# Optimization experiments

Measured on AMD Instinct MI355X. Metric: run time of the kernel, lower is better.

Reference implementation:

```python
import jax, jax.numpy as jnp
import numpy as np


def setup_inputs() -> dict:
    key = jax.random.key(0)
    ks = jax.random.split(key, 9)
    B, T, S, D = 4, 256, 256, 512
    scale = 1.0 / np.sqrt(D)
    inp = {
        "output": jax.random.normal(ks[0], (B, T, D), dtype=jnp.float32),
        "context": jax.random.normal(ks[1], (B, S, D), dtype=jnp.float32),
        "mask": jax.random.randint(ks[2], (B, S), 0, 2, dtype=jnp.int32),
        # learned params (nn.Linear stores y = x @ W.T + b; we store W.T directly)
        "Wq": jax.random.normal(ks[3], (D, D), dtype=jnp.float32) * scale,
        "bq": jax.random.normal(ks[4], (D,), dtype=jnp.float32) * scale,
        "Wc": jax.random.normal(ks[5], (D, D), dtype=jnp.float32) * scale,
        "v": jax.random.normal(ks[6], (D,), dtype=jnp.float32) * scale,
        "Wout": jax.random.normal(ks[7], (2 * D, D), dtype=jnp.float32) * scale,
        "bout": jax.random.normal(ks[8], (D,), dtype=jnp.float32) * scale,
    }
    return inp


def reference(output, context, mask, Wq, bq, Wc, v, Wout, bout):
    # output: (B, T, D) decoder states; context: (B, S, D) encoder states
    wq = jnp.einsum("btd,de->bte", output, Wq) + bq          # (B, T, D)
    uh = jnp.einsum("bsd,de->bse", context, Wc)               # (B, S, D)
    # additive score: v . tanh(wq + uh), broadcast over (T, S)
    wquh = jnp.tanh(wq[:, :, None, :] + uh[:, None, :, :])    # (B, T, S, D)
    score = jnp.einsum("btsd,d->bts", wquh, v)                # (B, T, S)
    # masked softmax exactly as the torch code: max over ALL positions,
    # then zero out masked entries (mask==1 means masked) and renormalize.
    max_by_row = jnp.max(score, axis=-1, keepdims=True)
    keep = (1.0 - mask.astype(score.dtype))[:, None, :]       # (B, 1, S)
    attn = jnp.exp(score - max_by_row) * keep
    attn = attn / jnp.sum(attn, axis=-1, keepdims=True)       # (B, T, S)
    mix = jnp.einsum("bts,bsd->btd", attn, context)           # (B, T, D)
    combined = jnp.concatenate([mix, output], axis=-1)        # (B, T, 2D)
    out = jnp.einsum("btf,fd->btd", combined, Wout) + bout    # (B, T, D)
    return out, attn
```

## Files before the change

### kernel.cpp

```cpp
#include <hip/hip_runtime.h>
#include <hip/hip_bf16.h>

#define B_ 4
#define T_ 256
#define S_ 256
#define D_ 512
#define TB 2

typedef __bf16 bf16x8 __attribute__((ext_vector_type(8)));
typedef float  floatx4 __attribute__((ext_vector_type(4)));

#define C2F 2.885390081777926f

static __device__ __forceinline__ unsigned short f2bf(float x) {
    __hip_bfloat16 h = __float2bfloat16(x);
    return *reinterpret_cast<unsigned short*>(&h);
}
static __device__ __forceinline__ float asf(unsigned int u) {
    float f; __builtin_memcpy(&f, &u, 4); return f;
}


__global__ __launch_bounds__(256) void prep(
    const float* __restrict__ output, const float* __restrict__ context,
    const float* __restrict__ Wq, const float* __restrict__ Wc,
    const float* __restrict__ Wout,
    unsigned short* __restrict__ out_f, unsigned short* __restrict__ ctx_f,
    unsigned short* __restrict__ Wq_f, unsigned short* __restrict__ Wc_f,
    unsigned short* __restrict__ WoT_f, unsigned short* __restrict__ WoB_f)
{
    const int tid = threadIdx.x;
    const int z = blockIdx.z;

    if (z >= 4) {
        const float* src = (z == 4) ? output : context;
        unsigned short* dst = (z == 4) ? out_f : ctx_f;
        const int bid  = blockIdx.y * 16 + blockIdx.x;
        const int tile = bid * 4 + (tid >> 6);
        const int lane = tid & 63;
        const int mblk = tile >> 4, kblk = tile & 15;
        const float* s = src + (size_t)(mblk * 16 + (lane & 15)) * 512
                             + kblk * 32 + (lane >> 4) * 8;
        float4 a = *(const float4*)s;
        float4 b = *(const float4*)(s + 4);
        uint4 pk;
        pk.x = (unsigned)f2bf(a.x) | ((unsigned)f2bf(a.y) << 16);
        pk.y = (unsigned)f2bf(a.z) | ((unsigned)f2bf(a.w) << 16);
        pk.z = (unsigned)f2bf(b.x) | ((unsigned)f2bf(b.y) << 16);
        pk.w = (unsigned)f2bf(b.z) | ((unsigned)f2bf(b.w) << 16);
        *(uint4*)(dst + (size_t)tile * 512 + lane * 8) = pk;
        return;
    }

    const float* W; unsigned short* WF; int krow0;
    if      (z == 0) { W = Wq;   WF = Wq_f;  krow0 = 0;   }
    else if (z == 1) { W = Wc;   WF = Wc_f;  krow0 = 0;   }
    else if (z == 2) { W = Wout; WF = WoT_f; krow0 = 0;   }
    else             { W = Wout; WF = WoB_f; krow0 = 512; }

    const int n0 = blockIdx.x * 32;
    const int k0 = blockIdx.y * 32;

    __shared__ float tile[32][33];
    const int c = tid & 31, r = tid >> 5;
    #pragma unroll
    for (int i = 0; i < 4; ++i)
        tile[r + 8 * i][c] = W[(size_t)(krow0 + k0 + r + 8 * i) * 512 + n0 + c];
    __syncthreads();
    #pragma unroll
    for (int i = 0; i < 4; ++i) {
        const int n = n0 + r + 8 * i;
        const int k = k0 + c;
        const int tl = (n >> 4) * 16 + (k >> 5);
        const int ln = (n & 15) | (((k >> 3) & 3) << 4);
        WF[((size_t)tl * 64 + ln) * 8 + (k & 7)] = f2bf(tile[c][r + 8 * i]);
    }
}

struct GArgs {
    const unsigned short* Af;
    const unsigned short* Bf;
    const float* aux;
    void* C;
    int mode;
};

__global__ __launch_bounds__(256) void gemm2(GArgs g0, GArgs g1, GArgs g2, GArgs g3)
{
    const int z = blockIdx.z;
    GArgs g = (z == 0) ? g0 : (z == 1) ? g1 : (z == 2) ? g2 : g3;

    const int tid  = threadIdx.x;
    const int wave = tid >> 6, lane = tid & 63;
    const int l15  = lane & 15, quad = lane >> 4;
    const int mblk = blockIdx.y * 4 + wave;
    const int nb0  = blockIdx.x * 2;

    const unsigned short* Ap  = g.Af + ((size_t)mblk * 16 * 64 + lane) * 8;
    const unsigned short* Bp0 = g.Bf + ((size_t)nb0 * 16 * 64 + lane) * 8;
    const unsigned short* Bp1 = Bp0 + (size_t)16 * 64 * 8;

    floatx4 acc[2];
    acc[0] = (floatx4){0.f, 0.f, 0.f, 0.f};
    acc[1] = (floatx4){0.f, 0.f, 0.f, 0.f};

    #pragma unroll 4
    for (int k = 0; k < 16; ++k) {
        bf16x8 a  = *(const bf16x8*)(Ap  + k * 512);
        bf16x8 b0 = *(const bf16x8*)(Bp0 + k * 512);
        bf16x8 b1 = *(const bf16x8*)(Bp1 + k * 512);
        acc[0] = __builtin_amdgcn_mfma_f32_16x16x32_bf16(a, b0, acc[0], 0, 0, 0);
        acc[1] = __builtin_amdgcn_mfma_f32_16x16x32_bf16(a, b1, acc[1], 0, 0, 0);
    }

    #pragma unroll
    for (int ni = 0; ni < 2; ++ni) {
        const int col = (nb0 + ni) * 16 + l15;
        const int rbase = mblk * 16 + quad * 4;
        if (g.mode == 3) {
            unsigned short* Cb = (unsigned short*)g.C;
            #pragma unroll
            for (int r = 0; r < 4; ++r) {
                int row = rbase + r, bb = row >> 8, ss = row & 255;
                Cb[((size_t)(bb * 64 + (col >> 3)) * 256 + ss) * 8 + (col & 7)]
                    = f2bf(C2F * acc[ni][r]);
            }
        } else if (g.mode == 5) {
            unsigned short* Cb = (unsigned short*)g.C;
            #pragma unroll
            for (int r = 0; r < 4; ++r)
                Cb[(size_t)(rbase + r) * 512 + col] = f2bf(acc[ni][r]);
        } else {
            float* Cf = (float*)g.C;
            float bv = g.aux ? g.aux[col] : 0.0f;
            #pragma unroll
            for (int r = 0; r < 4; ++r) {
                float val = acc[ni][r] + bv;
                if (g.mode == 1) val *= C2F;
                Cf[(size_t)(rbase + r) * 512 + col] = val;
            }
        }
    }
}

__global__ __launch_bounds__(1024) void attn_fused(
    const float* __restrict__ wqs,
    const unsigned short* __restrict__ uhb,
    const unsigned short* __restrict__ CWb,
    const float* __restrict__ OB,
    const int*   __restrict__ mask,
    const float* __restrict__ v,
    float* __restrict__ attn_out,
    float* __restrict__ out)
{
    const int bg  = blockIdx.x;
    const int b   = bg / (T_ / TB);
    const int t0  = (bg % (T_ / TB)) * TB;
    const int tid = threadIdx.x;
    const int s   = tid & 255;
    const int h   = tid >> 8;

    __shared__ float  w_s[TB][D_];
    __shared__ float  v_s[D_];
    __shared__ float2 part[4][256];
    __shared__ float2 wred[4];
    __shared__ float  a_s[TB][256];
    __shared__ float  mixp[4][TB][D_];

    if (tid < 512) {
        w_s[0][tid] = wqs[(size_t)(b * T_ + t0 + 0) * D_ + tid];
        w_s[1][tid] = wqs[(size_t)(b * T_ + t0 + 1) * D_ + tid];
        v_s[tid]    = v[tid];
    }
    __syncthreads();

    float acc0 = 0.f, acc1 = 0.f;
    const int dd0 = h * 16;
    const uint4* u4 = (const uint4*)(uhb + ((size_t)(b * 64 + dd0) * 256 + s) * 8);

    #pragma unroll 4
    for (int dd = 0; dd < 16; ++dd) {
        uint4 uu = u4[(size_t)dd * 256];
        float uf[8];
        uf[0] = asf(uu.x << 16); uf[1] = asf(uu.x & 0xffff0000u);
        uf[2] = asf(uu.y << 16); uf[3] = asf(uu.y & 0xffff0000u);
        uf[4] = asf(uu.z << 16); uf[5] = asf(uu.z & 0xffff0000u);
        uf[6] = asf(uu.w << 16); uf[7] = asf(uu.w & 0xffff0000u);

        const int dbase = (dd0 + dd) * 8;
        #pragma unroll
        for (int j = 0; j < 8; ++j) {
            float vv = v_s[dbase + j];
            float x0 = w_s[0][dbase + j] + uf[j];
            float x1 = w_s[1][dbase + j] + uf[j];
            float r0 = __builtin_amdgcn_rcpf(__builtin_amdgcn_exp2f(x0) + 1.0f);
            float r1 = __builtin_amdgcn_rcpf(__builtin_amdgcn_exp2f(x1) + 1.0f);
            acc0 = fmaf(vv, r0, acc0);
            acc1 = fmaf(vv, r1, acc1);
        }
    }
    part[h][s] = make_float2(acc0, acc1);
    __syncthreads();

    float p0 = 0.f, p1 = 0.f;
    if (tid < 256) {
        float A0 = part[0][tid].x + part[1][tid].x + part[2][tid].x + part[3][tid].x;
        float A1 = part[0][tid].y + part[1][tid].y + part[2][tid].y + part[3][tid].y;
        float keep = 1.0f - (float)mask[b * S_ + tid];
        p0 = __builtin_amdgcn_exp2f(-C2F * A0) * keep;
        p1 = __builtin_amdgcn_exp2f(-C2F * A1) * keep;
        float s0 = p0, s1 = p1;
        #pragma unroll
        for (int off = 1; off < 64; off <<= 1) {
            s0 += __shfl_xor(s0, off);
            s1 += __shfl_xor(s1, off);
        }
        if ((tid & 63) == 0) wred[tid >> 6] = make_float2(s0, s1);
    }
    __syncthreads();

    if (tid < 256) {
        float den0 = wred[0].x + wred[1].x + wred[2].x + wred[3].x;
        float den1 = wred[0].y + wred[1].y + wred[2].y + wred[3].y;
        float a0 = p0 * __builtin_amdgcn_rcpf(den0);
        float a1 = p1 * __builtin_amdgcn_rcpf(den1);
        attn_out[(size_t)(b * T_ + t0 + 0) * S_ + tid] = a0;
        attn_out[(size_t)(b * T_ + t0 + 1) * S_ + tid] = a1;
        a_s[0][tid] = a0;
        a_s[1][tid] = a1;
    }
    __syncthreads();

    const int d2 = tid & 255;
    const int sh = h * 64;
    const unsigned short* cw = CWb + ((size_t)(b * S_) + sh) * D_ + 2 * d2;
    float m[TB][2] = {};
    #pragma unroll 8
    for (int s2 = 0; s2 < 64; ++s2) {
        unsigned int cc = *(const unsigned int*)(cw + (size_t)s2 * D_);
        float c0 = asf(cc << 16), c1 = asf(cc & 0xffff0000u);
        #pragma unroll
        for (int t = 0; t < TB; ++t) {
            float a = a_s[t][sh + s2];
            m[t][0] = fmaf(a, c0, m[t][0]);
            m[t][1] = fmaf(a, c1, m[t][1]);
        }
    }
    #pragma unroll
    for (int t = 0; t < TB; ++t) {
        mixp[h][t][2 * d2]     = m[t][0];
        mixp[h][t][2 * d2 + 1] = m[t][1];
    }
    __syncthreads();

    {
        const int t = tid >> 9, d = tid & 511;
        size_t idx = (size_t)(b * T_ + t0 + t) * D_ + d;
        out[idx] = mixp[0][t][d] + mixp[1][t][d] + mixp[2][t][d] + mixp[3][t][d]
                 + OB[idx];
    }
}

extern "C" void kernel_launch(void* const* d_in, const int* in_sizes, int n_in,
                              void* d_out, int out_size, void* d_ws, size_t ws_size,
                              hipStream_t stream) {
    const float* output  = (const float*)d_in[0];
    const float* context = (const float*)d_in[1];
    const int*   mask    = (const int*)d_in[2];
    const float* Wq      = (const float*)d_in[3];
    const float* bq      = (const float*)d_in[4];
    const float* Wc      = (const float*)d_in[5];
    const float* v       = (const float*)d_in[6];
    const float* Wout    = (const float*)d_in[7];
    const float* bout    = (const float*)d_in[8];

    float* out  = (float*)d_out;
    float* attn = out + (size_t)B_ * T_ * D_;

    char* ws = (char*)d_ws;
    float* wqs           = (float*)ws;
    float* OB            = (float*)(ws + (2u << 20));
    unsigned short* uhb   = (unsigned short*)(ws + (4u << 20));
    unsigned short* out_f = (unsigned short*)(ws + (5u << 20));
    unsigned short* ctx_f = (unsigned short*)(ws + (6u << 20));
    unsigned short* Wq_f  = (unsigned short*)(ws + (7u << 20));
    unsigned short* Wc_f  = (unsigned short*)(ws + (7u << 20) + (512u << 10));
    unsigned short* WoT_f = (unsigned short*)(ws + (8u << 20));
    unsigned short* WoB_f = (unsigned short*)(ws + (8u << 20) + (512u << 10));
    unsigned short* CWb   = (unsigned short*)(ws + (9u << 20));

    dim3 blk(256);

    prep<<<dim3(16, 16, 6), blk, 0, stream>>>(
        output, context, Wq, Wc, Wout, out_f, ctx_f, Wq_f, Wc_f, WoT_f, WoB_f);

    GArgs gwq = { out_f, Wq_f,  bq,      wqs, 1 };
    GArgs guh = { ctx_f, Wc_f,  nullptr, uhb, 3 };
    GArgs gob = { out_f, WoB_f, bout,    OB,  4 };
    GArgs gcw = { ctx_f, WoT_f, nullptr, CWb, 5 };
    gemm2<<<dim3(16, 16, 4), blk, 0, stream>>>(gwq, guh, gob, gcw);

    attn_fused<<<dim3(B_ * T_ / TB), dim3(1024), 0, stream>>>(
        wqs, uhb, CWb, OB, mask, v, attn, out);
}
```

Measured before the change: 122.0 us.

## Fuse bf16 conversion into GEMM with LDS-staged 64x64 tiles, drop prep kernel

Removes the separate prep kernel that converted activations and weights to bf16 fragment layout. The GEMM now loads fp32 inputs directly, converts them to bf16 while staging into shared memory, and computes 64x64 tiles per block with a 2x2 wave layout. This saves one launch and the workspace round trip, at the cost of redundant conversion across blocks and uncoalesced strided weight-column loads with no double buffering.

Result: no change. 124.3 us (+1.8%).

```diff
diff --git a/kernel.cpp b/kernel.cpp
--- a/kernel.cpp
+++ b/kernel.cpp
@@ -20,124 +20,112 @@
     float f; __builtin_memcpy(&f, &u, 4); return f;
 }
 
-
-__global__ __launch_bounds__(256) void prep(
-    const float* __restrict__ output, const float* __restrict__ context,
-    const float* __restrict__ Wq, const float* __restrict__ Wc,
-    const float* __restrict__ Wout,
-    unsigned short* __restrict__ out_f, unsigned short* __restrict__ ctx_f,
-    unsigned short* __restrict__ Wq_f, unsigned short* __restrict__ Wc_f,
-    unsigned short* __restrict__ WoT_f, unsigned short* __restrict__ WoB_f)
-{
-    const int tid = threadIdx.x;
-    const int z = blockIdx.z;
-
-    if (z >= 4) {
-        const float* src = (z == 4) ? output : context;
-        unsigned short* dst = (z == 4) ? out_f : ctx_f;
-        const int bid  = blockIdx.y * 16 + blockIdx.x;
-        const int tile = bid * 4 + (tid >> 6);
-        const int lane = tid & 63;
-        const int mblk = tile >> 4, kblk = tile & 15;
-        const float* s = src + (size_t)(mblk * 16 + (lane & 15)) * 512
-                             + kblk * 32 + (lane >> 4) * 8;
-        float4 a = *(const float4*)s;
-        float4 b = *(const float4*)(s + 4);
-        uint4 pk;
-        pk.x = (unsigned)f2bf(a.x) | ((unsigned)f2bf(a.y) << 16);
-        pk.y = (unsigned)f2bf(a.z) | ((unsigned)f2bf(a.w) << 16);
-        pk.z = (unsigned)f2bf(b.x) | ((unsigned)f2bf(b.y) << 16);
-        pk.w = (unsigned)f2bf(b.z) | ((unsigned)f2bf(b.w) << 16);
-        *(uint4*)(dst + (size_t)tile * 512 + lane * 8) = pk;
-        return;
-    }
-
-    const float* W; unsigned short* WF; int krow0;
-    if      (z == 0) { W = Wq;   WF = Wq_f;  krow0 = 0;   }
-    else if (z == 1) { W = Wc;   WF = Wc_f;  krow0 = 0;   }
-    else if (z == 2) { W = Wout; WF = WoT_f; krow0 = 0;   }
-    else             { W = Wout; WF = WoB_f; krow0 = 512; }
-
-    const int n0 = blockIdx.x * 32;
-    const int k0 = blockIdx.y * 32;
-
-    __shared__ float tile[32][33];
-    const int c = tid & 31, r = tid >> 5;
-    #pragma unroll
-    for (int i = 0; i < 4; ++i)
-        tile[r + 8 * i][c] = W[(size_t)(krow0 + k0 + r + 8 * i) * 512 + n0 + c];
-    __syncthreads();
-    #pragma unroll
-    for (int i = 0; i < 4; ++i) {
-        const int n = n0 + r + 8 * i;
-        const int k = k0 + c;
-        const int tl = (n >> 4) * 16 + (k >> 5);
-        const int ln = (n & 15) | (((k >> 3) & 3) << 4);
-        WF[((size_t)tl * 64 + ln) * 8 + (k & 7)] = f2bf(tile[c][r + 8 * i]);
-    }
-}
-
-struct GArgs {
-    const unsigned short* Af;
-    const unsigned short* Bf;
+struct G3 {
+    const float* A;
+    const float* W;
+    int krow0;
     const float* aux;
     void* C;
     int mode;
 };
 
-__global__ __launch_bounds__(256) void gemm2(GArgs g0, GArgs g1, GArgs g2, GArgs g3)
+__global__ __launch_bounds__(256) void gemm3(G3 g0, G3 g1, G3 g2, G3 g3)
 {
     const int z = blockIdx.z;
-    GArgs g = (z == 0) ? g0 : (z == 1) ? g1 : (z == 2) ? g2 : g3;
+    G3 g = (z == 0) ? g0 : (z == 1) ? g1 : (z == 2) ? g2 : g3;
 
     const int tid  = threadIdx.x;
     const int wave = tid >> 6, lane = tid & 63;
     const int l15  = lane & 15, quad = lane >> 4;
-    const int mblk = blockIdx.y * 4 + wave;
-    const int nb0  = blockIdx.x * 2;
-
-    const unsigned short* Ap  = g.Af + ((size_t)mblk * 16 * 64 + lane) * 8;
-    const unsigned short* Bp0 = g.Bf + ((size_t)nb0 * 16 * 64 + lane) * 8;
-    const unsigned short* Bp1 = Bp0 + (size_t)16 * 64 * 8;
-
-    floatx4 acc[2];
-    acc[0] = (floatx4){0.f, 0.f, 0.f, 0.f};
-    acc[1] = (floatx4){0.f, 0.f, 0.f, 0.f};
-
-    #pragma unroll 4
-    for (int k = 0; k < 16; ++k) {
-        bf16x8 a  = *(const bf16x8*)(Ap  + k * 512);
-        bf16x8 b0 = *(const bf16x8*)(Bp0 + k * 512);
-        bf16x8 b1 = *(const bf16x8*)(Bp1 + k * 512);
-        acc[0] = __builtin_amdgcn_mfma_f32_16x16x32_bf16(a, b0, acc[0], 0, 0, 0);
-        acc[1] = __builtin_amdgcn_mfma_f32_16x16x32_bf16(a, b1, acc[1], 0, 0, 0);
-    }
-
+    const int wm   = wave >> 1, wn = wave & 1;
+    const int m0   = blockIdx.y * 64;
+    const int n0   = blockIdx.x * 64;
+
+    __shared__ unsigned short Af[4 * 64 * 8];
+    __shared__ unsigned short Bf[4 * 64 * 8];
+
+    const int sm  = tid >> 2, skq = tid & 3;
+    const int sn  = tid & 63, sk8 = (tid >> 6) * 8;
+
+    const float* Abase = g.A + (size_t)(m0 + sm) * 512 + skq * 8;
+    const float* Wbase = g.W + (size_t)(g.krow0 + sk8) * 512 + n0 + sn;
+
+    unsigned short* Awr = Af + ((size_t)(sm >> 4) * 64 + ((sm & 15) | (skq << 4))) * 8;
+    unsigned short* Bwr = Bf + ((size_t)(sn >> 4) * 64 + ((sn & 15) | ((sk8 >> 3) << 4))) * 8;
+
+    const unsigned short* Ard0 = Af + ((size_t)(wm * 2 + 0) * 64 + lane) * 8;
+    const unsigned short* Ard1 = Af + ((size_t)(wm * 2 + 1) * 64 + lane) * 8;
+    const unsigned short* Brd0 = Bf + ((size_t)(wn * 2 + 0) * 64 + lane) * 8;
+    const unsigned short* Brd1 = Bf + ((size_t)(wn * 2 + 1) * 64 + lane) * 8;
+
+    floatx4 acc[2][2];
     #pragma unroll
-    for (int ni = 0; ni < 2; ++ni) {
-        const int col = (nb0 + ni) * 16 + l15;
-        const int rbase = mblk * 16 + quad * 4;
-        if (g.mode == 3) {
-            unsigned short* Cb = (unsigned short*)g.C;
-            #pragma unroll
-            for (int r = 0; r < 4; ++r) {
-                int row = rbase + r, bb = row >> 8, ss = row & 255;
-                Cb[((size_t)(bb * 64 + (col >> 3)) * 256 + ss) * 8 + (col & 7)]
-                    = f2bf(C2F * acc[ni][r]);
-            }
-        } else if (g.mode == 5) {
-            unsigned short* Cb = (unsigned short*)g.C;
-            #pragma unroll
-            for (int r = 0; r < 4; ++r)
-                Cb[(size_t)(rbase + r) * 512 + col] = f2bf(acc[ni][r]);
-        } else {
-            float* Cf = (float*)g.C;
-            float bv = g.aux ? g.aux[col] : 0.0f;
-            #pragma unroll
-            for (int r = 0; r < 4; ++r) {
-                float val = acc[ni][r] + bv;
-                if (g.mode == 1) val *= C2F;
-                Cf[(size_t)(rbase + r) * 512 + col] = val;
+    for (int i = 0; i < 2; ++i)
+        #pragma unroll
+        for (int j = 0; j < 2; ++j) acc[i][j] = (floatx4){0.f, 0.f, 0.f, 0.f};
+
+    for (int chunk = 0; chunk < 16; ++chunk) {
+        const int k0 = chunk * 32;
+        float4 a0 = *(const float4*)(Abase + k0);
+        float4 a1 = *(const float4*)(Abase + k0 + 4);
+        float bcol[8];
+        #pragma unroll
+        for (int j = 0; j < 8; ++j)
+            bcol[j] = Wbase[(size_t)(k0 + j) * 512];
+
+        __syncthreads();
+        uint4 pa;
+        pa.x = (unsigned)f2bf(a0.x) | ((unsigned)f2bf(a0.y) << 16);
+        pa.y = (unsigned)f2bf(a0.z) | ((unsigned)f2bf(a0.w) << 16);
+        pa.z = (unsigned)f2bf(a1.x) | ((unsigned)f2bf(a1.y) << 16);
+        pa.w = (unsigned)f2bf(a1.z) | ((unsigned)f2bf(a1.w) << 16);
+        *(uint4*)Awr = pa;
+        uint4 pb;
+        pb.x = (unsigned)f2bf(bcol[0]) | ((unsigned)f2bf(bcol[1]) << 16);
+        pb.y = (unsigned)f2bf(bcol[2]) | ((unsigned)f2bf(bcol[3]) << 16);
+        pb.z = (unsigned)f2bf(bcol[4]) | ((unsigned)f2bf(bcol[5]) << 16);
+        pb.w = (unsigned)f2bf(bcol[6]) | ((unsigned)f2bf(bcol[7]) << 16);
+        *(uint4*)Bwr = pb;
+        __syncthreads();
+
+        bf16x8 fa0 = *(const bf16x8*)Ard0;
+        bf16x8 fa1 = *(const bf16x8*)Ard1;
+        bf16x8 fb0 = *(const bf16x8*)Brd0;
+        bf16x8 fb1 = *(const bf16x8*)Brd1;
+        acc[0][0] = __builtin_amdgcn_mfma_f32_16x16x32_bf16(fa0, fb0, acc[0][0], 0, 0, 0);
+        acc[0][1] = __builtin_amdgcn_mfma_f32_16x16x32_bf16(fa0, fb1, acc[0][1], 0, 0, 0);
+        acc[1][0] = __builtin_amdgcn_mfma_f32_16x16x32_bf16(fa1, fb0, acc[1][0], 0, 0, 0);
+        acc[1][1] = __builtin_amdgcn_mfma_f32_16x16x32_bf16(fa1, fb1, acc[1][1], 0, 0, 0);
+    }
+
+    #pragma unroll
+    for (int mi = 0; mi < 2; ++mi) {
+        #pragma unroll
+        for (int ni = 0; ni < 2; ++ni) {
+            const int col = n0 + wn * 32 + ni * 16 + l15;
+            const int rbase = m0 + wm * 32 + mi * 16 + quad * 4;
+            if (g.mode == 3) {
+                unsigned short* Cb = (unsigned short*)g.C;
+                #pragma unroll
+                for (int r = 0; r < 4; ++r) {
+                    int row = rbase + r, bb = row >> 8, ss = row & 255;
+                    Cb[((size_t)(bb * 64 + (col >> 3)) * 256 + ss) * 8 + (col & 7)]
+                        = f2bf(C2F * acc[mi][ni][r]);
+                }
+            } else if (g.mode == 5) {
+                unsigned short* Cb = (unsigned short*)g.C;
+                #pragma unroll
+                for (int r = 0; r < 4; ++r)
+                    Cb[(size_t)(rbase + r) * 512 + col] = f2bf(acc[mi][ni][r]);
+            } else {
+                float* Cf = (float*)g.C;
+                float bv = g.aux ? g.aux[col] : 0.0f;
+                #pragma unroll
+                for (int r = 0; r < 4; ++r) {
+                    float val = acc[mi][ni][r] + bv;
+                    if (g.mode == 1) val *= C2F;
+                    Cf[(size_t)(rbase + r) * 512 + col] = val;
+                }
             }
         }
     }
@@ -278,27 +266,16 @@
     float* attn = out + (size_t)B_ * T_ * D_;
 
     char* ws = (char*)d_ws;
-    float* wqs           = (float*)ws;
-    float* OB            = (float*)(ws + (2u << 20));
-    unsigned short* uhb   = (unsigned short*)(ws + (4u << 20));
-    unsigned short* out_f = (unsigned short*)(ws + (5u << 20));
-    unsigned short* ctx_f = (unsigned short*)(ws + (6u << 20));
-    unsigned short* Wq_f  = (unsigned short*)(ws + (7u << 20));
-    unsigned short* Wc_f  = (unsigned short*)(ws + (7u << 20) + (512u << 10));
-    unsigned short* WoT_f = (unsigned short*)(ws + (8u << 20));
-    unsigned short* WoB_f = (unsigned short*)(ws + (8u << 20) + (512u << 10));
-    unsigned short* CWb   = (unsigned short*)(ws + (9u << 20));
-
-    dim3 blk(256);
-
-    prep<<<dim3(16, 16, 6), blk, 0, stream>>>(
-        output, context, Wq, Wc, Wout, out_f, ctx_f, Wq_f, Wc_f, WoT_f, WoB_f);
-
-    GArgs gwq = { out_f, Wq_f,  bq,      wqs, 1 };
-    GArgs guh = { ctx_f, Wc_f,  nullptr, uhb, 3 };
-    GArgs gob = { out_f, WoB_f, bout,    OB,  4 };
-    GArgs gcw = { ctx_f, WoT_f, nullptr, CWb, 5 };
-    gemm2<<<dim3(16, 16, 4), blk, 0, stream>>>(gwq, guh, gob, gcw);
+    float* wqs          = (float*)ws;
+    float* OB           = (float*)(ws + (2u << 20));
+    unsigned short* uhb = (unsigned short*)(ws + (4u << 20));
+    unsigned short* CWb = (unsigned short*)(ws + (5u << 20));
+
+    G3 gwq = { output,  Wq,     0, bq,      wqs, 1 };
+    G3 guh = { context, Wc,     0, nullptr, uhb, 3 };
+    G3 gob = { output,  Wout, 512, bout,    OB,  4 };
+    G3 gcw = { context, Wout,   0, nullptr, CWb, 5 };
+    gemm3<<<dim3(8, 16, 4), dim3(256), 0, stream>>>(gwq, guh, gob, gcw);
 
     attn_fused<<<dim3(B_ * T_ / TB), dim3(1024), 0, stream>>>(
         wqs, uhb, CWb, OB, mask, v, attn, out);
```
